# Kernel tuning notes

Hardware: AMD Instinct MI355X
Metric: run time of the kernel (lower is better)

## Reference

```python
import jax, jax.numpy as jnp
import numpy as np

RADIUS = 0.2
K = 32  # num_neighbors


def setup_inputs() -> dict:
    key = jax.random.key(0)
    k1, k2, k3 = jax.random.split(key, 3)
    points_xyz = jax.random.uniform(k1, (2, 16384, 3), dtype=jnp.float32)
    center_xyz = jax.random.uniform(k2, (2, 2048, 3), dtype=jnp.float32)
    features = jax.random.normal(k3, (2, 64, 16384), dtype=jnp.float32)
    return {"points_xyz": points_xyz, "center_xyz": center_xyz, "features": features}


def _ball_query(center_xyz, points_xyz, k, radius):
    # squared distances (B, G, N) via ||c||^2 + ||p||^2 - 2 c.p (avoids (B,G,N,3) temp)
    c2 = jnp.sum(center_xyz * center_xyz, axis=-1)  # (B, G)
    p2 = jnp.sum(points_xyz * points_xyz, axis=-1)  # (B, N)
    cp = jnp.einsum('bgd,bnd->bgn', center_xyz, points_xyz)
    d2 = c2[:, :, None] + p2[:, None, :] - 2.0 * cp  # (B, G, N)
    n = points_xyz.shape[1]
    # key = point index if inside ball else sentinel N; first-K-in-ball == K smallest keys
    keys = jnp.where(d2 < radius * radius, jnp.arange(n, dtype=jnp.int32), n)
    neg_vals, _ = jax.lax.top_k(-keys, k)
    idx = -neg_vals  # (B, G, K) ascending point indices, sentinel n if <k found
    first = idx[..., :1]
    # pad missing slots with first found index (CUDA ball_query semantics), 0 if none
    idx = jnp.where(idx < n, idx, jnp.where(first < n, first, 0))
    return idx


def reference(points_xyz, center_xyz, features):
    idx = _ball_query(center_xyz, points_xyz, K, RADIUS)  # (B, G, K) int32
    gather = jax.vmap(lambda f, i: f[:, i])  # (C, N), (G, K) -> (C, G, K)
    grouped_xyz = gather(jnp.swapaxes(points_xyz, 1, 2), idx)  # (B, 3, G, K)
    # relative_xyz then normalize_xyz
    grouped_xyz = (grouped_xyz - jnp.swapaxes(center_xyz, 1, 2)[..., None]) / RADIUS
    grouped_features = gather(features, idx)  # (B, C, G, K)
    return grouped_xyz, grouped_features
```

## Files before the change

kernel.cpp:

```cpp
#include <hip/hip_runtime.h>
#include <hip/hip_bf16.h>

constexpr int NPTS = 16384;
constexpr int NCTR = 2048;
constexpr int NCH  = 64;
constexpr int KK   = 32;
constexpr int NB   = 2;
#define R2 0.04f

__global__ __launch_bounds__(256) void prep_kernel(
    const float* __restrict__ points,
    const float* __restrict__ feats,
    float* __restrict__ featsT,
    float4* __restrict__ packed)
{
#pragma clang fp contract(off)
    __shared__ float tile[64][65];

    if (blockIdx.x < 512) {
        const int b  = blockIdx.x >> 8;
        const int n0 = (blockIdx.x & 255) * 64;
        const int t  = threadIdx.x;
        const int nl = t & 63;
        const int q  = t >> 6;

        const float* fb = feats + (size_t)b * NCH * NPTS;
#pragma unroll
        for (int r = 0; r < 16; ++r) {
            int c = r * 4 + q;
            tile[c][nl] = fb[(size_t)c * NPTS + n0 + nl];
        }
        __syncthreads();
        float* ftb = featsT + ((size_t)b * NPTS + n0) * NCH;
#pragma unroll
        for (int r = 0; r < 16; ++r) {
            int n = r * 4 + q;
            ftb[(size_t)n * NCH + nl] = tile[nl][n];
        }
        return;
    }

    const int tid = (blockIdx.x - 512) * 256 + threadIdx.x;
#pragma unroll
    for (int s = 0; s < 4; ++s) {
        const int i = tid + s * 8192;
        const float x = points[3 * i + 0];
        const float y = points[3 * i + 1];
        const float z = points[3 * i + 2];
        const float p2 = (x * x + y * y) + z * z;
        packed[i] = make_float4(x + x, y + y, z + z, p2);
    }
}

__global__ __launch_bounds__(256, 4) void query_group(
    const float4* __restrict__ packed,
    const float* __restrict__ centers,
    const float* __restrict__ featsT,
    float* __restrict__ out_xyz,
    float* __restrict__ out_feat)
{
#pragma clang fp contract(off)
    __shared__ int   s_idx[4][KK];
    __shared__ float s_f[4][16][68];

    const int wave = threadIdx.x >> 6;
    const int lane = threadIdx.x & 63;
    const int cg   = blockIdx.x * 4 + wave;
    const int b    = cg >> 11;
    const int g    = cg & (NCTR - 1);

    const float4* pk = packed + (size_t)b * NPTS;
    const float* cc = centers + (size_t)cg * 3;
    const float cx = cc[0], cy = cc[1], cz = cc[2];
    const float c2 = (cx * cx + cy * cy) + cz * cz;

    int* idxs = s_idx[wave];

    float4 cur[8], nxt[8];
#pragma unroll
    for (int j = 0; j < 8; ++j) cur[j] = pk[j * 64 + lane];
    int cnt = 0;
    for (int base = 0; base < NPTS; base += 512) {
        const int nbb = (base + 512 < NPTS) ? base + 512 : 0;
#pragma unroll
        for (int j = 0; j < 8; ++j) nxt[j] = pk[nbb + j * 64 + lane];
#pragma unroll
        for (int j = 0; j < 8; ++j) {
            const float4 v = cur[j];
            const float cp2 = (cx * v.x + cy * v.y) + cz * v.z;
            const float d2 = (c2 + v.w) - cp2;
            const bool hit = d2 < R2;
            const unsigned long long m = __ballot(hit);
            if (hit) {
                const int slot = cnt + __popcll(m & ((1ull << lane) - 1ull));
                if (slot < KK) idxs[slot] = base + j * 64 + lane;
            }
            cnt += (int)__popcll(m);
        }
        if (cnt >= KK) break;
#pragma unroll
        for (int j = 0; j < 8; ++j) cur[j] = nxt[j];
    }

    const int cpd = cnt < KK ? cnt : KK;
    const int first = (cnt > 0) ? idxs[0] : 0;
    if (lane < KK) {
        const int id = (lane < cpd) ? idxs[lane] : first;
        idxs[lane] = id;
        const float4 v = pk[id];
        const float px = 0.5f * v.x, py = 0.5f * v.y, pz = 0.5f * v.z;
        const size_t ob = (((size_t)b * 3 + 0) * NCTR + g) * KK + lane;
        out_xyz[ob + (size_t)0 * NCTR * KK] = (px - cx) / 0.2f;
        out_xyz[ob + (size_t)1 * NCTR * KK] = (py - cy) / 0.2f;
        out_xyz[ob + (size_t)2 * NCTR * KK] = (pz - cz) / 0.2f;
    }

    float (*sf)[68] = s_f[wave];
    const int li = lane & 15, r = lane >> 4;
    const int kqL = lane & 3, c0 = lane >> 2;
    const float* ftb = featsT + (size_t)b * NPTS * NCH;
    const size_t ob = ((size_t)b * NCH * NCTR + g) * KK;
#pragma unroll
    for (int pass = 0; pass < 2; ++pass) {
        const int k0 = pass * 16;
#pragma unroll
        for (int i = 0; i < 4; ++i) {
            const int kl = i * 4 + r;
            const float4 v = *((const float4*)(ftb + (size_t)idxs[k0 + kl] * NCH) + li);
            *(float4*)&sf[kl][4 * li] = v;
        }
#pragma unroll
        for (int p = 0; p < 4; ++p) {
            const int c = c0 + 16 * p;
            float4 w;
            w.x = sf[4 * kqL + 0][c];
            w.y = sf[4 * kqL + 1][c];
            w.z = sf[4 * kqL + 2][c];
            w.w = sf[4 * kqL + 3][c];
            *(float4*)(out_feat + ob + (size_t)c * NCTR * KK + k0 + 4 * kqL) = w;
        }
    }
}

__global__ __launch_bounds__(256) void ballquery_group(
    const float* __restrict__ points, const float* __restrict__ centers,
    const float* __restrict__ feats, float* __restrict__ out_xyz,
    float* __restrict__ out_feat)
{
#pragma clang fp contract(off)
    __shared__ int   s_idx[4][KK];
    __shared__ float s_f[4][KK][65];
    const int wave = threadIdx.x >> 6, lane = threadIdx.x & 63;
    const int cg = blockIdx.x * 4 + wave;
    const int b = cg >> 11, g = cg & (NCTR - 1);
    const float* pb = points + (size_t)b * NPTS * 3;
    const float* cc = centers + (size_t)cg * 3;
    const float cx = cc[0], cy = cc[1], cz = cc[2];
    const float c2 = (cx * cx + cy * cy) + cz * cz;
    int* idxs = s_idx[wave];
    int cnt = 0;
    for (int base = 0; base < NPTS; base += 64) {
        const int i = base + lane;
        const float px = pb[i * 3 + 0], py = pb[i * 3 + 1], pz = pb[i * 3 + 2];
        const float p2 = (px * px + py * py) + pz * pz;
        const float cp = (cx * px + cy * py) + cz * pz;
        const float d2 = (c2 + p2) - 2.0f * cp;
        const bool hit = d2 < R2;
        const unsigned long long m = __ballot(hit);
        if (hit) {
            const int slot = cnt + __popcll(m & ((1ull << lane) - 1ull));
            if (slot < KK) idxs[slot] = i;
        }
        cnt += (int)__popcll(m);
        if (cnt >= KK) break;
    }
    __syncthreads();
    const int cpd = cnt < KK ? cnt : KK;
    const int first = (cnt > 0) ? idxs[0] : 0;
    if (lane < KK) idxs[lane] = (lane < cpd) ? idxs[lane] : first;
    __syncthreads();
    if (lane < KK) {
        const int id = idxs[lane];
        const float px = pb[id * 3 + 0], py = pb[id * 3 + 1], pz = pb[id * 3 + 2];
        const size_t ob = (((size_t)b * 3 + 0) * NCTR + g) * KK + lane;
        out_xyz[ob + (size_t)0 * NCTR * KK] = (px - cx) / 0.2f;
        out_xyz[ob + (size_t)1 * NCTR * KK] = (py - cy) / 0.2f;
        out_xyz[ob + (size_t)2 * NCTR * KK] = (pz - cz) / 0.2f;
    }
    float (*sf)[65] = s_f[wave];
    const float* fb = feats + (size_t)b * NCH * NPTS;
    for (int k = 0; k < KK; ++k) {
        const int id = idxs[k];
        sf[k][lane] = fb[(size_t)lane * NPTS + id];
    }
    __syncthreads();
    const int k = lane & 31, ch = lane >> 5;
    const size_t ob = ((size_t)b * NCH * NCTR + g) * KK;
#pragma unroll
    for (int cc2 = 0; cc2 < 32; ++cc2) {
        const int c = cc2 * 2 + ch;
        out_feat[ob + (size_t)c * NCTR * KK + k] = sf[k][c];
    }
}

extern "C" void kernel_launch(void* const* d_in, const int* in_sizes, int n_in,
                              void* d_out, int out_size, void* d_ws, size_t ws_size,
                              hipStream_t stream) {
    const float* points  = (const float*)d_in[0];
    const float* centers = (const float*)d_in[1];
    const float* feats   = (const float*)d_in[2];

    float* out      = (float*)d_out;
    float* out_xyz  = out;
    float* out_feat = out + (size_t)NB * 3 * NCTR * KK;

    const size_t ftBytes = (size_t)NB * NPTS * NCH * sizeof(float);
    const size_t pkBytes = (size_t)NB * NPTS * 4 * sizeof(float);

    if (ws_size >= ftBytes + pkBytes) {
        float*  featsT = (float*)d_ws;
        float4* packed = (float4*)((char*)d_ws + ftBytes);
        prep_kernel<<<544, 256, 0, stream>>>(points, feats, featsT, packed);
        query_group<<<(NB * NCTR) / 4, 256, 0, stream>>>(
            packed, centers, featsT, out_xyz, out_feat);
    } else {
        ballquery_group<<<(NB * NCTR) / 4, 256, 0, stream>>>(
            points, centers, feats, out_xyz, out_feat);
    }
}
```

Measured before the change: 86.65 us.

## Use one-wave blocks per center and batch ballots before slot assignment

The query kernel now launches one 64-thread block per center instead of four waves per block. Blocks become finer-grained and waves no longer share an allocation unit, so a wave that finishes its search early frees its slot sooner. The ball-query loop evaluates all eight ballots first and then assigns slots in a second pass, cutting the serial dependency between compare and ballot. The feature gather loads all 32 neighbours in one shot before transposing. The risk is higher block-launch overhead from four times as many blocks, and the per-block LDS changes.

```diff
diff --git a/kernel.cpp b/kernel.cpp
--- a/kernel.cpp
+++ b/kernel.cpp
@@ -52,7 +52,7 @@
     }
 }
 
-__global__ __launch_bounds__(256, 4) void query_group(
+__global__ __launch_bounds__(64, 4) void query_group(
     const float4* __restrict__ packed,
     const float* __restrict__ centers,
     const float* __restrict__ featsT,
@@ -60,12 +60,11 @@
     float* __restrict__ out_feat)
 {
 #pragma clang fp contract(off)
-    __shared__ int   s_idx[4][KK];
-    __shared__ float s_f[4][16][68];
-
-    const int wave = threadIdx.x >> 6;
-    const int lane = threadIdx.x & 63;
-    const int cg   = blockIdx.x * 4 + wave;
+    __shared__ int   idxs[KK];
+    __shared__ float sf[KK][68];
+
+    const int lane = threadIdx.x;
+    const int cg   = blockIdx.x;
     const int b    = cg >> 11;
     const int g    = cg & (NCTR - 1);
 
@@ -74,29 +73,33 @@
     const float cx = cc[0], cy = cc[1], cz = cc[2];
     const float c2 = (cx * cx + cy * cy) + cz * cz;
 
-    int* idxs = s_idx[wave];
-
     float4 cur[8], nxt[8];
 #pragma unroll
     for (int j = 0; j < 8; ++j) cur[j] = pk[j * 64 + lane];
     int cnt = 0;
+    const unsigned long long lmask = (1ull << lane) - 1ull;
     for (int base = 0; base < NPTS; base += 512) {
         const int nbb = (base + 512 < NPTS) ? base + 512 : 0;
 #pragma unroll
         for (int j = 0; j < 8; ++j) nxt[j] = pk[nbb + j * 64 + lane];
+
+        unsigned long long m[8];
 #pragma unroll
         for (int j = 0; j < 8; ++j) {
             const float4 v = cur[j];
             const float cp2 = (cx * v.x + cy * v.y) + cz * v.z;
-            const float d2 = (c2 + v.w) - cp2;
-            const bool hit = d2 < R2;
-            const unsigned long long m = __ballot(hit);
-            if (hit) {
-                const int slot = cnt + __popcll(m & ((1ull << lane) - 1ull));
+            m[j] = __ballot((c2 + v.w) - cp2 < R2);
+        }
+        int run = cnt;
+#pragma unroll
+        for (int j = 0; j < 8; ++j) {
+            if ((m[j] >> lane) & 1ull) {
+                const int slot = run + __popcll(m[j] & lmask);
                 if (slot < KK) idxs[slot] = base + j * 64 + lane;
             }
-            cnt += (int)__popcll(m);
-        }
+            run += (int)__popcll(m[j]);
+        }
+        cnt = run;
         if (cnt >= KK) break;
 #pragma unroll
         for (int j = 0; j < 8; ++j) cur[j] = nxt[j];
@@ -115,29 +118,29 @@
         out_xyz[ob + (size_t)2 * NCTR * KK] = (pz - cz) / 0.2f;
     }
 
-    float (*sf)[68] = s_f[wave];
     const int li = lane & 15, r = lane >> 4;
-    const int kqL = lane & 3, c0 = lane >> 2;
     const float* ftb = featsT + (size_t)b * NPTS * NCH;
+#pragma unroll
+    for (int i = 0; i < 8; ++i) {
+        const int k = i * 4 + r;
+        const float4 v = *((const float4*)(ftb + (size_t)idxs[k] * NCH) + li);
+        *(float4*)&sf[k][4 * li] = v;
+    }
+
+    const int kq = lane & 3, c0 = lane >> 2;
     const size_t ob = ((size_t)b * NCH * NCTR + g) * KK;
 #pragma unroll
-    for (int pass = 0; pass < 2; ++pass) {
-        const int k0 = pass * 16;
-#pragma unroll
-        for (int i = 0; i < 4; ++i) {
-            const int kl = i * 4 + r;
-            const float4 v = *((const float4*)(ftb + (size_t)idxs[k0 + kl] * NCH) + li);
-            *(float4*)&sf[kl][4 * li] = v;
-        }
+    for (int h = 0; h < 2; ++h) {
 #pragma unroll
         for (int p = 0; p < 4; ++p) {
             const int c = c0 + 16 * p;
+            const int k = 16 * h + 4 * kq;
             float4 w;
-            w.x = sf[4 * kqL + 0][c];
-            w.y = sf[4 * kqL + 1][c];
-            w.z = sf[4 * kqL + 2][c];
-            w.w = sf[4 * kqL + 3][c];
-            *(float4*)(out_feat + ob + (size_t)c * NCTR * KK + k0 + 4 * kqL) = w;
+            w.x = sf[k + 0][c];
+            w.y = sf[k + 1][c];
+            w.z = sf[k + 2][c];
+            w.w = sf[k + 3][c];
+            *(float4*)(out_feat + ob + (size_t)c * NCTR * KK + k) = w;
         }
     }
 }
@@ -221,7 +224,7 @@
         float*  featsT = (float*)d_ws;
         float4* packed = (float4*)((char*)d_ws + ftBytes);
         prep_kernel<<<544, 256, 0, stream>>>(points, feats, featsT, packed);
-        query_group<<<(NB * NCTR) / 4, 256, 0, stream>>>(
+        query_group<<<NB * NCTR, 64, 0, stream>>>(
             packed, centers, featsT, out_xyz, out_feat);
     } else {
         ballquery_group<<<(NB * NCTR) / 4, 256, 0, stream>>>(
```

After: 86.40 us. About the same (-0.3%).
